# Kernel tuning notes

Hardware: AMD Instinct MI355X
Metric: run time of the kernel (lower is better)

The kernel has to match this reference:

```python
import jax, jax.numpy as jnp
import numpy as np

B, S, F, E = 8, 2048, 512, 512

def setup_inputs() -> dict:
    key = jax.random.key(0)
    k1, k2, k3, k4 = jax.random.split(key, 4)
    x = jax.random.normal(k1, (B, S, F), dtype=jnp.float32)
    # nn.Linear(feat, embed, bias=False): y = x @ W.T; store W as [F, E] already transposed
    scale = 1.0 / np.sqrt(F)
    Wq = jax.random.uniform(k2, (F, E), dtype=jnp.float32, minval=-scale, maxval=scale)
    Wk = jax.random.uniform(k3, (F, E), dtype=jnp.float32, minval=-scale, maxval=scale)
    Wv = jax.random.uniform(k4, (F, E), dtype=jnp.float32, minval=-scale, maxval=scale)
    return {"x": x, "Wq": Wq, "Wk": Wk, "Wv": Wv}

def reference(x, Wq, Wk, Wv):
    # QKV projections: [B, S, E]
    Q = jnp.einsum('bsf,fe->bse', x, Wq)
    K = jnp.einsum('bsf,fe->bse', x, Wk)
    V = jnp.einsum('bsf,fe->bse', x, Wv)
    # scores: [B, S, S], scaled by sqrt(E)
    scores = jnp.einsum('bqe,bke->bqk', Q, K) / jnp.sqrt(jnp.asarray(Q.shape[-1], Q.dtype))
    attn = jax.nn.softmax(scores, axis=-1)
    return jnp.einsum('bqk,bke->bqe', attn, V)
```

## Files before the change

### kernel.cpp

```cpp
#include <hip/hip_runtime.h>
#include <hip/hip_bf16.h>
#include <stdint.h>

#define B_ 8
#define S_ 2048
#define F_ 512
#define E_ 512

typedef short bf16x8 __attribute__((ext_vector_type(8)));
typedef float f32x4 __attribute__((ext_vector_type(4)));

__device__ __forceinline__ f32x4 mfma16(bf16x8 a, bf16x8 b, f32x4 c) {
  return __builtin_amdgcn_mfma_f32_16x16x32_bf16(a, b, c, 0, 0, 0);
}

__device__ __forceinline__ void gll16(const void* g, void* l) {
  __builtin_amdgcn_global_load_lds(
      (const __attribute__((address_space(1))) void*)g,
      (__attribute__((address_space(3))) void*)l, 16, 0, 0);
}

constexpr float QSCALE = 0.0441941738f * 1.44269504f;

__global__ void xconv_kernel(const float* __restrict__ x,
                             __hip_bfloat16* __restrict__ xb) {
  int i = (blockIdx.x * 256 + threadIdx.x) * 8;
  float4 a = *(const float4*)(x + i);
  float4 b = *(const float4*)(x + i + 4);
  union { __hip_bfloat16 h[8]; uint4 u; } cv;
  cv.h[0] = __float2bfloat16(a.x);
  cv.h[1] = __float2bfloat16(a.y);
  cv.h[2] = __float2bfloat16(a.z);
  cv.h[3] = __float2bfloat16(a.w);
  cv.h[4] = __float2bfloat16(b.x);
  cv.h[5] = __float2bfloat16(b.y);
  cv.h[6] = __float2bfloat16(b.z);
  cv.h[7] = __float2bfloat16(b.w);
  *(uint4*)(xb + i) = cv.u;
}

__global__ void wtrans_kernel(const float* __restrict__ wq,
                              const float* __restrict__ wk,
                              const float* __restrict__ wv,
                              __hip_bfloat16* __restrict__ wt) {
  __shared__ float t[32][33];
  const float* w = (blockIdx.z == 0) ? wq : (blockIdx.z == 1 ? wk : wv);
  __hip_bfloat16* o = wt + (size_t)blockIdx.z * F_ * E_;
  int e0 = blockIdx.x * 32, f0 = blockIdx.y * 32;
  int tx = threadIdx.x, ty = threadIdx.y;
#pragma unroll
  for (int i = 0; i < 4; i++)
    t[ty + 8 * i][tx] = w[(size_t)(f0 + ty + 8 * i) * E_ + e0 + tx];
  __syncthreads();
#pragma unroll
  for (int i = 0; i < 4; i++)
    o[(size_t)(e0 + ty + 8 * i) * F_ + f0 + tx] = __float2bfloat16(t[tx][ty + 8 * i]);
}

__global__ __launch_bounds__(256, 2) void qkvg_kernel(
    const __hip_bfloat16* __restrict__ xb, const __hip_bfloat16* __restrict__ wt,
    __hip_bfloat16* __restrict__ Qb, __hip_bfloat16* __restrict__ Kb,
    __hip_bfloat16* __restrict__ Vt) {
  __shared__ __hip_bfloat16 Al[2][128][64] __attribute__((aligned(16)));
  __shared__ __hip_bfloat16 Bl[2][128][64] __attribute__((aligned(16)));

  int tid = threadIdx.x;
  int lane = tid & 63, w = tid >> 6;
  int el = lane & 15, g = lane >> 4;
  int r7 = el & 7;
  int m0 = blockIdx.x * 128, n0 = blockIdx.y * 128, z = blockIdx.z;
  const __hip_bfloat16* wz = wt + (size_t)z * F_ * E_;
  int wr = w >> 1, wc = w & 1;

  int srcoff = (((lane & 7) ^ ((lane >> 3) & 7)) << 3);
  auto stage = [&](int kk, int bf) {
#pragma unroll
    for (int i = 0; i < 4; i++) {
      int row = w * 32 + i * 8 + (lane >> 3);
      gll16(xb + (size_t)(m0 + row) * F_ + kk * 64 + srcoff, &Al[bf][w * 32 + i * 8][0]);
      gll16(wz + (size_t)(n0 + row) * F_ + kk * 64 + srcoff, &Bl[bf][w * 32 + i * 8][0]);
    }
  };

  f32x4 acc[4][4] = {};
  stage(0, 0);
  asm volatile("s_waitcnt vmcnt(0)" ::: "memory");
  __syncthreads();

  for (int kk = 0; kk < 8; ++kk) {
    int bf = kk & 1;
    if (kk < 7) stage(kk + 1, bf ^ 1);
#pragma unroll
    for (int ks = 0; ks < 2; ++ks) {
      bf16x8 av[4], bv[4];
#pragma unroll
      for (int mi = 0; mi < 4; mi++)
        av[mi] = *(const bf16x8*)((const char*)&Al[bf][0][0] +
                                  (wr * 64 + mi * 16 + el) * 128 +
                                  (((ks * 4 + g) ^ r7) << 4));
#pragma unroll
      for (int ni = 0; ni < 4; ni++)
        bv[ni] = *(const bf16x8*)((const char*)&Bl[bf][0][0] +
                                  (wc * 64 + ni * 16 + el) * 128 +
                                  (((ks * 4 + g) ^ r7) << 4));
#pragma unroll
      for (int mi = 0; mi < 4; mi++)
#pragma unroll
        for (int ni = 0; ni < 4; ni++)
          acc[mi][ni] = mfma16(av[mi], bv[ni], acc[mi][ni]);
    }
    asm volatile("s_waitcnt vmcnt(0)" ::: "memory");
    __syncthreads();
  }

  float sc = (z == 0) ? QSCALE : 1.0f;
#pragma unroll
  for (int mi = 0; mi < 4; mi++)
#pragma unroll
    for (int ni = 0; ni < 4; ni++) {
      int mB = m0 + wr * 64 + mi * 16 + g * 4;
      int n = n0 + wc * 64 + ni * 16 + el;
      if (z == 2) {
        union { __hip_bfloat16 h[4]; uint2 u; } pk;
#pragma unroll
        for (int r = 0; r < 4; r++) pk.h[r] = __float2bfloat16(acc[mi][ni][r]);
        int b = mB >> 11, sl = mB & 2047;
        *(uint2*)&Vt[(size_t)b * E_ * S_ + (size_t)n * S_ + sl] = pk.u;
      } else {
#pragma unroll
        for (int r = 0; r < 4; r++) {
          __hip_bfloat16 v = __float2bfloat16(acc[mi][ni][r] * sc);
          if (z == 0) Qb[(size_t)(mB + r) * E_ + n] = v;
          else Kb[(size_t)(mB + r) * E_ + n] = v;
        }
      }
    }
}

__global__ __launch_bounds__(256, 2) void qkv_kernel(
    const float* __restrict__ x, const __hip_bfloat16* __restrict__ wt,
    __hip_bfloat16* __restrict__ Qb, __hip_bfloat16* __restrict__ Kb,
    __hip_bfloat16* __restrict__ Vt) {
  __shared__ __hip_bfloat16 Al[2][128][72];
  __shared__ __hip_bfloat16 Bl[2][128][72];
  int tid = threadIdx.x;
  int lane = tid & 63, w = tid >> 6;
  int el = lane & 15, g = lane >> 4;
  int m0 = blockIdx.x * 128, n0 = blockIdx.y * 128, z = blockIdx.z;
  const __hip_bfloat16* wz = wt + (size_t)z * F_ * E_;
  int wr = w >> 1, wc = w & 1;
  float4 fa[8];
  uint4 vb[4];
  auto load = [&](int kk) {
#pragma unroll
    for (int c = 0; c < 4; c++) {
      int id = tid + 256 * c;
      int row = id >> 3, k8 = (id & 7) * 8;
      const float* s = x + (size_t)(m0 + row) * F_ + kk * 64 + k8;
      fa[2 * c] = *(const float4*)s;
      fa[2 * c + 1] = *(const float4*)(s + 4);
      vb[c] = *(const uint4*)(wz + (size_t)(n0 + row) * F_ + kk * 64 + k8);
    }
  };
  auto store_lds = [&](int bf) {
#pragma unroll
    for (int c = 0; c < 4; c++) {
      int id = tid + 256 * c;
      int row = id >> 3, k8 = (id & 7) * 8;
      union { __hip_bfloat16 h[8]; uint4 u; } cv;
      cv.h[0] = __float2bfloat16(fa[2 * c].x);
      cv.h[1] = __float2bfloat16(fa[2 * c].y);
      cv.h[2] = __float2bfloat16(fa[2 * c].z);
      cv.h[3] = __float2bfloat16(fa[2 * c].w);
      cv.h[4] = __float2bfloat16(fa[2 * c + 1].x);
      cv.h[5] = __float2bfloat16(fa[2 * c + 1].y);
      cv.h[6] = __float2bfloat16(fa[2 * c + 1].z);
      cv.h[7] = __float2bfloat16(fa[2 * c + 1].w);
      *(uint4*)&Al[bf][row][k8] = cv.u;
      *(uint4*)&Bl[bf][row][k8] = vb[c];
    }
  };
  f32x4 acc[4][4] = {};
  load(0);
  store_lds(0);
  __syncthreads();
  for (int kk = 0; kk < 8; ++kk) {
    int bf = kk & 1;
    if (kk < 7) load(kk + 1);
#pragma unroll
    for (int ks = 0; ks < 2; ++ks) {
      bf16x8 av[4], bv[4];
#pragma unroll
      for (int mi = 0; mi < 4; mi++)
        av[mi] = *(const bf16x8*)((const char*)&Al[bf][0][0] +
                                  (wr * 64 + mi * 16 + el) * 144 + (ks * 32 + g * 8) * 2);
#pragma unroll
      for (int ni = 0; ni < 4; ni++)
        bv[ni] = *(const bf16x8*)((const char*)&Bl[bf][0][0] +
                                  (wc * 64 + ni * 16 + el) * 144 + (ks * 32 + g * 8) * 2);
#pragma unroll
      for (int mi = 0; mi < 4; mi++)
#pragma unroll
        for (int ni = 0; ni < 4; ni++)
          acc[mi][ni] = mfma16(av[mi], bv[ni], acc[mi][ni]);
    }
    if (kk < 7) store_lds(bf ^ 1);
    __syncthreads();
  }
  float sc = (z == 0) ? QSCALE : 1.0f;
#pragma unroll
  for (int mi = 0; mi < 4; mi++)
#pragma unroll
    for (int ni = 0; ni < 4; ni++)
#pragma unroll
      for (int r = 0; r < 4; r++) {
        int m = m0 + wr * 64 + mi * 16 + g * 4 + r;
        int n = n0 + wc * 64 + ni * 16 + el;
        __hip_bfloat16 v = __float2bfloat16(acc[mi][ni][r] * sc);
        if (z == 0) Qb[(size_t)m * E_ + n] = v;
        else if (z == 1) Kb[(size_t)m * E_ + n] = v;
        else {
          int b = m >> 11, sl = m & 2047;
          Vt[(size_t)b * E_ * S_ + (size_t)n * S_ + sl] = v;
        }
      }
}

template <int MODE>
__global__ __launch_bounds__(256, 2) void attn_kernel(
    const __hip_bfloat16* __restrict__ Qb, const __hip_bfloat16* __restrict__ Kb,
    const __hip_bfloat16* __restrict__ Vt, float* __restrict__ out,
    float* __restrict__ part1, float* __restrict__ Ls, float* __restrict__ Ms) {
  __shared__ __hip_bfloat16 Kl[32][512] __attribute__((aligned(16)));
  __shared__ __hip_bfloat16 Vl[512][32] __attribute__((aligned(16)));
  __shared__ __hip_bfloat16 Pl[4][16][40] __attribute__((aligned(16)));
  __shared__ float Fac[64] __attribute__((aligned(16)));
  __shared__ float Lf[64] __attribute__((aligned(16)));
  __shared__ int Flag[4];

  int tid = threadIdx.x;
  int lane = tid & 63, w = tid >> 6;
  int el = lane & 15, g = lane >> 4, x7 = lane & 7;
  int bx = blockIdx.x;
  int batch = bx & 7, qt = (bx >> 3) & 31;
  int half = MODE ? (bx >> 8) : 0;
  int nt = MODE ? 32 : 64;
  int tbase = half * 32;
  int q0 = qt * 64;

  bf16x8 qf[16];
  {
    const __hip_bfloat16* qptr =
        Qb + (size_t)(batch * S_ + q0 + w * 16 + el) * E_ + g * 8;
#pragma unroll
    for (int s = 0; s < 16; s++) qf[s] = *(const bf16x8*)(qptr + 32 * s);
  }

  f32x4 o[4][8] = {};
  float m_run = -INFINITY, l_run = 0.f;

  const char* kbase_g = (const char*)(Kb + (size_t)batch * S_ * E_);
  const char* vbase_g = (const char*)(Vt + (size_t)batch * E_ * S_);
  int vsrc_lane = (lane >> 2) * (S_ * 2) + 16 * ((lane & 3) ^ ((lane >> 3) & 3));

  auto stage = [&](int t) {
#pragma unroll
    for (int i = 0; i < 8; i++) {
      int row = w * 8 + i;
      const char* src =
          kbase_g + ((size_t)(t * 32 + row) * 512 + 8 * (lane ^ i)) * 2;
      gll16(src, &Kl[row][0]);
    }
#pragma unroll
    for (int i = 0; i < 8; i++) {
      int eb = (w * 8 + i) * 16;
      const char* src = vbase_g + (size_t)eb * (S_ * 2) + vsrc_lane + t * 64;
      gll16(src, &Vl[eb][0]);
    }
  };

  int ka0 = el * 1024 + ((g ^ x7) << 4);
  int ka1 = el * 1024 + (((4 + g) ^ x7) << 4);
  int vbase_l = el * 64 + ((g ^ ((el >> 1) & 3)) << 4);

  stage(tbase);
  asm volatile("s_waitcnt vmcnt(0)" ::: "memory");
  __syncthreads();

  for (int i = 0; i < nt; ++i) {
    const char* kl = (const char*)&Kl[0][0];
    f32x4 st[2] = {};
    __builtin_amdgcn_s_setprio(1);
#pragma unroll
    for (int s = 0; s < 16; s++) {
      int base = ((s & 1) ? ka1 : ka0) + (s >> 1) * 128;
#pragma unroll
      for (int f = 0; f < 2; f++) {
        bf16x8 kf = *(const bf16x8*)(kl + base + f * 16384);
        st[f] = mfma16(kf, qf[s], st[f]);
      }
    }
    __builtin_amdgcn_s_setprio(0);
    float vmax = st[0][0];
#pragma unroll
    for (int r = 1; r < 4; r++) vmax = fmaxf(vmax, st[0][r]);
#pragma unroll
    for (int r = 0; r < 4; r++) vmax = fmaxf(vmax, st[1][r]);
    vmax = fmaxf(vmax, __shfl_xor(vmax, 16));
    vmax = fmaxf(vmax, __shfl_xor(vmax, 32));
    int resc = __any(vmax > m_run + 8.0f) ? 1 : 0;
    float fac = 1.0f;
    if (resc) {
      float m_new = fmaxf(m_run, vmax);
      fac = exp2f(m_run - m_new);
      l_run *= fac;
      m_run = m_new;
    }
    if (g == 0) Fac[w * 16 + el] = fac;
    if (lane == 0) Flag[w] = resc;
    float p[8];
    float rs = 0.f;
#pragma unroll
    for (int f = 0; f < 2; f++)
#pragma unroll
      for (int r = 0; r < 4; r++) {
        float e2 = exp2f(st[f][r] - m_run);
        p[4 * f + r] = e2;
        rs += e2;
      }
    rs += __shfl_xor(rs, 16);
    rs += __shfl_xor(rs, 32);
    l_run += rs;
#pragma unroll
    for (int f = 0; f < 2; f++) {
      union { __hip_bfloat16 h[4]; uint2 u; } pk;
      pk.h[0] = __float2bfloat16(p[4 * f + 0]);
      pk.h[1] = __float2bfloat16(p[4 * f + 1]);
      pk.h[2] = __float2bfloat16(p[4 * f + 2]);
      pk.h[3] = __float2bfloat16(p[4 * f + 3]);
      *(uint2*)((char*)&Pl[w][0][0] + el * 80 + 32 * f + 8 * g) = pk.u;
    }
    __syncthreads();
    int fl = Flag[0] | Flag[1] | Flag[2] | Flag[3];
    bf16x8 pa[4];
#pragma unroll
    for (int qb = 0; qb < 4; qb++)
      pa[qb] = *(const bf16x8*)((const char*)&Pl[qb][0][0] + el * 80 + g * 16);
    if (fl) {
#pragma unroll
      for (int qb = 0; qb < 4; qb++) {
        f32x4 f4 = *(const f32x4*)&Fac[qb * 16 + g * 4];
#pragma unroll
        for (int nb = 0; nb < 8; nb++) {
          o[qb][nb][0] *= f4[0];
          o[qb][nb][1] *= f4[1];
          o[qb][nb][2] *= f4[2];
          o[qb][nb][3] *= f4[3];
        }
      }
    }
    const char* vl = (const char*)&Vl[0][0];
#pragma unroll
    for (int h = 0; h < 2; h++) {
      bf16x8 vf[4];
#pragma unroll
      for (int j = 0; j < 4; j++)
        vf[j] = *(const bf16x8*)(vl + (w * 8 + h * 4 + j) * 1024 + vbase_l);
      __builtin_amdgcn_s_setprio(1);
#pragma unroll
      for (int qb = 0; qb < 4; qb++)
#pragma unroll
        for (int j = 0; j < 4; j++)
          o[qb][h * 4 + j] = mfma16(pa[qb], vf[j], o[qb][h * 4 + j]);
      __builtin_amdgcn_s_setprio(0);
    }
    __syncthreads();
    if (i + 1 < nt) {
      stage(tbase + i + 1);
      asm volatile("s_waitcnt vmcnt(0)" ::: "memory");
      __syncthreads();
    }
  }

  if (MODE == 0) {
    if (g == 0) Lf[w * 16 + el] = l_run;
    __syncthreads();
    float* ob = out + (size_t)(batch * S_ + q0) * E_ + w * 128;
#pragma unroll
    for (int qb = 0; qb < 4; qb++) {
      f32x4 l4 = *(const f32x4*)&Lf[qb * 16 + g * 4];
      float li[4];
#pragma unroll
      for (int r = 0; r < 4; r++) li[r] = 1.0f / l4[r];
#pragma unroll
      for (int nb = 0; nb < 8; nb++)
#pragma unroll
        for (int r = 0; r < 4; r++)
          ob[(size_t)(qb * 16 + g * 4 + r) * E_ + nb * 16 + el] = o[qb][nb][r] * li[r];
    }
  } else {
    float* dst = (half == 0) ? out : part1;
    float* ob = dst + (size_t)(batch * S_ + q0) * E_ + w * 128;
#pragma unroll
    for (int qb = 0; qb < 4; qb++)
#pragma unroll
      for (int nb = 0; nb < 8; nb++)
#pragma unroll
        for (int r = 0; r < 4; r++)
          ob[(size_t)(qb * 16 + g * 4 + r) * E_ + nb * 16 + el] = o[qb][nb][r];
    if (g == 0) {
      int idx = half * (B_ * S_) + batch * S_ + q0 + w * 16 + el;
      Ls[idx] = l_run;
      Ms[idx] = m_run;
    }
  }
}

__global__ void merge_kernel(float* __restrict__ out,
                             const float* __restrict__ part1,
                             const float* __restrict__ Ls,
                             const float* __restrict__ Ms) {
  int idx = blockIdx.x * 256 + threadIdx.x;
  int row = idx >> 7;
  int c4 = (idx & 127) * 4;
  float l0 = Ls[row], m0 = Ms[row];
  float l1 = Ls[B_ * S_ + row], m1 = Ms[B_ * S_ + row];
  float m = fmaxf(m0, m1);
  float w0 = exp2f(m0 - m), w1 = exp2f(m1 - m);
  float inv = 1.0f / (l0 * w0 + l1 * w1);
  size_t off = (size_t)row * E_ + c4;
  float4 a = *(const float4*)(out + off);
  float4 b = *(const float4*)(part1 + off);
  float4 r;
  r.x = (a.x * w0 + b.x * w1) * inv;
  r.y = (a.y * w0 + b.y * w1) * inv;
  r.z = (a.z * w0 + b.z * w1) * inv;
  r.w = (a.w * w0 + b.w * w1) * inv;
  *(float4*)(out + off) = r;
}

extern "C" void kernel_launch(void* const* d_in, const int* in_sizes, int n_in,
                              void* d_out, int out_size, void* d_ws, size_t ws_size,
                              hipStream_t stream) {
  const float* x = (const float*)d_in[0];
  const float* wq = (const float*)d_in[1];
  const float* wk = (const float*)d_in[2];
  const float* wv = (const float*)d_in[3];
  float* out = (float*)d_out;

  char* ws = (char*)d_ws;
  __hip_bfloat16* wt = (__hip_bfloat16*)ws;
  __hip_bfloat16* Qb = (__hip_bfloat16*)(ws + (size_t)3 * F_ * E_ * 2);
  __hip_bfloat16* Kb = Qb + (size_t)B_ * S_ * E_;
  __hip_bfloat16* Vt = Kb + (size_t)B_ * S_ * E_;
  __hip_bfloat16* xb = Vt + (size_t)B_ * S_ * E_;
  float* part1 = (float*)(ws + (size_t)3 * F_ * E_ * 2 + (size_t)3 * B_ * S_ * E_ * 2 +
                          (size_t)B_ * S_ * F_ * 2);
  float* Ls = part1 + (size_t)B_ * S_ * E_;
  float* Ms = Ls + 2 * B_ * S_;

  size_t need_bfx = (size_t)3 * F_ * E_ * 2 + (size_t)3 * B_ * S_ * E_ * 2 +
                    (size_t)B_ * S_ * F_ * 2;
  size_t need_split = need_bfx + (size_t)B_ * S_ * E_ * 4 + 4 * B_ * S_ * 4;
  bool bfx = (ws_size >= need_bfx);
  bool split = (ws_size >= need_split);

  dim3 b0(32, 8), g0(16, 16, 3);
  wtrans_kernel<<<g0, b0, 0, stream>>>(wq, wk, wv, wt);

  dim3 g1(128, 4, 3);
  if (bfx) {
    xconv_kernel<<<(B_ * S_ * F_) / (256 * 8), 256, 0, stream>>>(x, xb);
    qkvg_kernel<<<g1, 256, 0, stream>>>(xb, wt, Qb, Kb, Vt);
  } else {
    qkv_kernel<<<g1, 256, 0, stream>>>(x, wt, Qb, Kb, Vt);
  }

  if (split) {
    attn_kernel<1><<<512, 256, 0, stream>>>(Qb, Kb, Vt, out, part1, Ls, Ms);
    merge_kernel<<<(B_ * S_ * E_ / 4) / 256, 256, 0, stream>>>(out, part1, Ls, Ms);
  } else {
    attn_kernel<0><<<256, 256, 0, stream>>>(Qb, Kb, Vt, out, nullptr, nullptr, nullptr);
  }
}
```

Measured before the change: 207.7 us.

## Give each wave its own query rows across full E in PV to drop barrier

Each wave now owns its 16 query rows across all 512 output columns in the P·V product, instead of splitting output columns across waves and sharing P tiles. The wave's own P tile can then be read back without a block-wide barrier, and softmax rescale factors and row sums move through lane shuffles rather than shared memory. This removes one __syncthreads per KV tile and the Fac, Flag and Lf shared arrays. In exchange each wave reads the whole V tile from LDS per step. Launch bounds for MODE 0 drop to one block per SM, allowing more registers.

```diff
diff --git a/kernel.cpp b/kernel.cpp
--- a/kernel.cpp
+++ b/kernel.cpp
@@ -227,16 +227,13 @@
 }
 
 template <int MODE>
-__global__ __launch_bounds__(256, 2) void attn_kernel(
+__global__ __launch_bounds__(256, MODE ? 2 : 1) void attn_kernel(
     const __hip_bfloat16* __restrict__ Qb, const __hip_bfloat16* __restrict__ Kb,
     const __hip_bfloat16* __restrict__ Vt, float* __restrict__ out,
     float* __restrict__ part1, float* __restrict__ Ls, float* __restrict__ Ms) {
   __shared__ __hip_bfloat16 Kl[32][512] __attribute__((aligned(16)));
   __shared__ __hip_bfloat16 Vl[512][32] __attribute__((aligned(16)));
   __shared__ __hip_bfloat16 Pl[4][16][40] __attribute__((aligned(16)));
-  __shared__ float Fac[64] __attribute__((aligned(16)));
-  __shared__ float Lf[64] __attribute__((aligned(16)));
-  __shared__ int Flag[4];
 
   int tid = threadIdx.x;
   int lane = tid & 63, w = tid >> 6;
@@ -246,17 +243,16 @@
   int half = MODE ? (bx >> 8) : 0;
   int nt = MODE ? 32 : 64;
   int tbase = half * 32;
-  int q0 = qt * 64;
+  int q0 = qt * 64 + w * 16;
 
   bf16x8 qf[16];
   {
-    const __hip_bfloat16* qptr =
-        Qb + (size_t)(batch * S_ + q0 + w * 16 + el) * E_ + g * 8;
+    const __hip_bfloat16* qptr = Qb + (size_t)(batch * S_ + q0 + el) * E_ + g * 8;
 #pragma unroll
     for (int s = 0; s < 16; s++) qf[s] = *(const bf16x8*)(qptr + 32 * s);
   }
 
-  f32x4 o[4][8] = {};
+  f32x4 o[32] = {};
   float m_run = -INFINITY, l_run = 0.f;
 
   const char* kbase_g = (const char*)(Kb + (size_t)batch * S_ * E_);
@@ -308,16 +304,19 @@
     for (int r = 0; r < 4; r++) vmax = fmaxf(vmax, st[1][r]);
     vmax = fmaxf(vmax, __shfl_xor(vmax, 16));
     vmax = fmaxf(vmax, __shfl_xor(vmax, 32));
-    int resc = __any(vmax > m_run + 8.0f) ? 1 : 0;
-    float fac = 1.0f;
-    if (resc) {
+    if (__any(vmax > m_run + 8.0f)) {
       float m_new = fmaxf(m_run, vmax);
-      fac = exp2f(m_run - m_new);
+      float fac = exp2f(m_run - m_new);
+      float fo[4];
+#pragma unroll
+      for (int r = 0; r < 4; r++) fo[r] = __shfl(fac, g * 4 + r);
+#pragma unroll
+      for (int ni = 0; ni < 32; ni++) {
+        o[ni][0] *= fo[0]; o[ni][1] *= fo[1]; o[ni][2] *= fo[2]; o[ni][3] *= fo[3];
+      }
       l_run *= fac;
       m_run = m_new;
     }
-    if (g == 0) Fac[w * 16 + el] = fac;
-    if (lane == 0) Flag[w] = resc;
     float p[8];
     float rs = 0.f;
 #pragma unroll
@@ -340,40 +339,16 @@
       pk.h[3] = __float2bfloat16(p[4 * f + 3]);
       *(uint2*)((char*)&Pl[w][0][0] + el * 80 + 32 * f + 8 * g) = pk.u;
     }
-    __syncthreads();
-    int fl = Flag[0] | Flag[1] | Flag[2] | Flag[3];
-    bf16x8 pa[4];
-#pragma unroll
-    for (int qb = 0; qb < 4; qb++)
-      pa[qb] = *(const bf16x8*)((const char*)&Pl[qb][0][0] + el * 80 + g * 16);
-    if (fl) {
-#pragma unroll
-      for (int qb = 0; qb < 4; qb++) {
-        f32x4 f4 = *(const f32x4*)&Fac[qb * 16 + g * 4];
-#pragma unroll
-        for (int nb = 0; nb < 8; nb++) {
-          o[qb][nb][0] *= f4[0];
-          o[qb][nb][1] *= f4[1];
-          o[qb][nb][2] *= f4[2];
-          o[qb][nb][3] *= f4[3];
-        }
-      }
-    }
+    asm volatile("s_waitcnt lgkmcnt(0)" ::: "memory");
+    bf16x8 pa = *(const bf16x8*)((const char*)&Pl[w][0][0] + el * 80 + g * 16);
     const char* vl = (const char*)&Vl[0][0];
-#pragma unroll
-    for (int h = 0; h < 2; h++) {
-      bf16x8 vf[4];
-#pragma unroll
-      for (int j = 0; j < 4; j++)
-        vf[j] = *(const bf16x8*)(vl + (w * 8 + h * 4 + j) * 1024 + vbase_l);
-      __builtin_amdgcn_s_setprio(1);
-#pragma unroll
-      for (int qb = 0; qb < 4; qb++)
-#pragma unroll
-        for (int j = 0; j < 4; j++)
-          o[qb][h * 4 + j] = mfma16(pa[qb], vf[j], o[qb][h * 4 + j]);
-      __builtin_amdgcn_s_setprio(0);
-    }
+    __builtin_amdgcn_s_setprio(1);
+#pragma unroll
+    for (int ni = 0; ni < 32; ni++) {
+      bf16x8 vf = *(const bf16x8*)(vl + vbase_l + ni * 1024);
+      o[ni] = mfma16(pa, vf, o[ni]);
+    }
+    __builtin_amdgcn_s_setprio(0);
     __syncthreads();
     if (i + 1 < nt) {
       stage(tbase + i + 1);
@@ -383,33 +358,28 @@
   }
 
   if (MODE == 0) {
-    if (g == 0) Lf[w * 16 + el] = l_run;
-    __syncthreads();
-    float* ob = out + (size_t)(batch * S_ + q0) * E_ + w * 128;
-#pragma unroll
-    for (int qb = 0; qb < 4; qb++) {
-      f32x4 l4 = *(const f32x4*)&Lf[qb * 16 + g * 4];
-      float li[4];
-#pragma unroll
-      for (int r = 0; r < 4; r++) li[r] = 1.0f / l4[r];
-#pragma unroll
-      for (int nb = 0; nb < 8; nb++)
-#pragma unroll
-        for (int r = 0; r < 4; r++)
-          ob[(size_t)(qb * 16 + g * 4 + r) * E_ + nb * 16 + el] = o[qb][nb][r] * li[r];
-    }
+    float linv[4];
+#pragma unroll
+    for (int r = 0; r < 4; r++) {
+      float lr = __shfl(l_run, g * 4 + r);
+      linv[r] = 1.0f / lr;
+    }
+    float* ob = out + (size_t)(batch * S_ + q0 + g * 4) * E_ + el;
+#pragma unroll
+    for (int ni = 0; ni < 32; ni++)
+#pragma unroll
+      for (int r = 0; r < 4; r++)
+        ob[(size_t)r * E_ + ni * 16] = o[ni][r] * linv[r];
   } else {
     float* dst = (half == 0) ? out : part1;
-    float* ob = dst + (size_t)(batch * S_ + q0) * E_ + w * 128;
-#pragma unroll
-    for (int qb = 0; qb < 4; qb++)
-#pragma unroll
-      for (int nb = 0; nb < 8; nb++)
-#pragma unroll
-        for (int r = 0; r < 4; r++)
-          ob[(size_t)(qb * 16 + g * 4 + r) * E_ + nb * 16 + el] = o[qb][nb][r];
+    float* ob = dst + (size_t)(batch * S_ + q0 + g * 4) * E_ + el;
+#pragma unroll
+    for (int ni = 0; ni < 32; ni++)
+#pragma unroll
+      for (int r = 0; r < 4; r++)
+        ob[(size_t)r * E_ + ni * 16] = o[ni][r];
     if (g == 0) {
-      int idx = half * (B_ * S_) + batch * S_ + q0 + w * 16 + el;
+      int idx = half * (B_ * S_) + batch * S_ + q0 + el;
       Ls[idx] = l_run;
       Ms[idx] = m_run;
     }
```

After: 185.3 us. 10.8% less time.
